# Performance work log

Hardware: AMD Instinct MI355X
Metric: run time of the kernel (lower is better)

The kernel has to match this reference:

```python
import jax, jax.numpy as jnp
import numpy as np

N, NC, E, S = 65536, 24576, 524288, 256
VAR_DIM, H1, H2, H3, H4 = 6, 128, 128, 256, 128
THRE, EPS = 0.7, 1e-5


def _bn(x, g, b):
    # BatchNorm1d, training-mode batch statistics (biased var), dropout treated as identity
    mu = x.mean(0)
    v = x.var(0)
    return (x - mu) * jax.lax.rsqrt(v + EPS) * g + b


def _gcn_sparse(h, src, dst, ew, W, b):
    # PyG GCNConv with edge weights: add self-loops (weight 1), symmetric normalization
    n = h.shape[0]
    loop = jnp.arange(n)
    s = jnp.concatenate([src, loop])
    d = jnp.concatenate([dst, loop])
    w = jnp.concatenate([ew, jnp.ones((n,), h.dtype)])
    deg = jax.ops.segment_sum(w, d, num_segments=n)
    dinv = jnp.where(deg > 0, jax.lax.rsqrt(deg), 0.0)
    norm = dinv[s] * w * dinv[d]
    xw = h @ W.T  # [n, out]
    out = jax.ops.segment_sum(norm[:, None] * xw[s], d, num_segments=n)
    return out + b


def _gcn_dense(h, A, W, b):
    # GCNConv on a dense binary adjacency (no edge weights), self-loops + sym norm
    n = h.shape[0]
    A_hat = A + jnp.eye(n, dtype=h.dtype)
    deg = A_hat.sum(0)
    dinv = jnp.where(deg > 0, jax.lax.rsqrt(deg), 0.0)
    return dinv[:, None] * (A_hat.T @ ((h @ W.T) * dinv[:, None])) + b


def setup_inputs() -> dict:
    key = jax.random.key(0)
    ks = jax.random.split(key, 10)

    def w(k, o, i):
        return jax.random.normal(k, (o, i), jnp.float32) / np.float32(np.sqrt(i))

    x = jax.random.normal(ks[0], (N, VAR_DIM), jnp.float32)
    edge_attr = jax.random.uniform(ks[1], (E,), jnp.float32)
    scen_adj = jax.random.uniform(ks[2], (S, S), jnp.float32)
    edge_index = jax.random.randint(ks[3], (2, E), 0, N)
    batch = jnp.arange(N) // (N // S)  # sorted node->graph ids, 256 nodes per graph
    mark = jnp.concatenate([jnp.ones((NC,), jnp.int32), jnp.zeros((N - NC,), jnp.int32)])
    return {
        "x": x, "edge_attr": edge_attr, "scen_adj": scen_adj,
        "mlp_var_w": w(ks[4], H1, VAR_DIM), "mlp_var_b": jnp.zeros((H1,), jnp.float32),
        "mlp_con_w": w(ks[5], H1, 1), "mlp_con_b": jnp.zeros((H1,), jnp.float32),
        "conv1_w": w(ks[6], H2, H1), "conv1_b": jnp.zeros((H2,), jnp.float32),
        "conv2_w": w(ks[7], H3, H2), "conv2_b": jnp.zeros((H3,), jnp.float32),
        "conv3_w": w(ks[8], H4, H3), "conv3_b": jnp.zeros((H4,), jnp.float32),
        "bn1_g": jnp.ones((H1,), jnp.float32), "bn1_b": jnp.zeros((H1,), jnp.float32),
        "bn2_g": jnp.ones((H2,), jnp.float32), "bn2_b": jnp.zeros((H2,), jnp.float32),
        "bn3_g": jnp.ones((H3,), jnp.float32), "bn3_b": jnp.zeros((H3,), jnp.float32),
        "mark": mark, "edge_index": edge_index, "batch": batch, "n_con": NC,
    }


def reference(x, edge_attr, scen_adj, mlp_var_w, mlp_var_b, mlp_con_w, mlp_con_b,
              conv1_w, conv1_b, conv2_w, conv2_b, conv3_w, conv3_b,
              bn1_g, bn1_b, bn2_g, bn2_b, bn3_g, bn3_b,
              mark, edge_index, batch, n_con):
    nc = int(n_con)  # mark layout: first nc nodes are constraints (mark==1), rest vars
    con_feat = jnp.tanh(x[:nc, 0:1] @ mlp_con_w.T + mlp_con_b)
    var_feat = jnp.tanh(x[nc:] @ mlp_var_w.T + mlp_var_b)
    h = jnp.concatenate([con_feat, var_feat], axis=0)  # [N, H1], con-first as in torch cat
    h = _bn(h, bn1_g, bn1_b)  # dropout = identity (eval)
    h = _gcn_sparse(h, edge_index[0], edge_index[1], edge_attr, conv1_w, conv1_b)
    h = jnp.tanh(_bn(h, bn2_g, bn2_b))
    s = scen_adj.shape[0]
    sums = jax.ops.segment_sum(h, batch, num_segments=s)
    cnt = jax.ops.segment_sum(jnp.ones((h.shape[0],), h.dtype), batch, num_segments=s)
    pooled = sums / jnp.maximum(cnt, 1.0)[:, None]  # global_mean_pool -> [S, H2]
    A = (scen_adj >= THRE).astype(h.dtype)  # filter_adj + unweighted edges
    f = jnp.tanh(_bn(_gcn_dense(pooled, A, conv2_w, conv2_b), bn3_g, bn3_b))
    feat = jnp.tanh(_gcn_dense(f, A, conv3_w, conv3_b))
    return feat, feat.mean(0)
```

## Files before the change

kernel.cpp:

```cpp
#include <hip/hip_runtime.h>
#include <hip/hip_bf16.h>
#include <cstddef>

#define N_NODES 65536
#define N_EDGES 524288
#define S_GRAPH 256
#define BN_EPS 1e-5f
#define THRE 0.7f

typedef __hip_bfloat16 bf16;
typedef unsigned int uint32;
typedef unsigned char uchar;
typedef unsigned short ushort16;
typedef __attribute__((ext_vector_type(8))) short short8;
typedef __attribute__((ext_vector_type(4))) float f32x4;

__device__ __forceinline__ float blo(uint32 u) { return __uint_as_float(u << 16); }
__device__ __forceinline__ float bhi(uint32 u) { return __uint_as_float(u & 0xffff0000u); }

__device__ __forceinline__ uint32 packbf(float a, float b)
{
    bf16 ha = __float2bfloat16(a), hb = __float2bfloat16(b);
    unsigned short ua, ub;
    __builtin_memcpy(&ua, &ha, 2); __builtin_memcpy(&ub, &hb, 2);
    return (uint32)ua | ((uint32)ub << 16);
}

__device__ __forceinline__ float ftanh(float x)
{
    float e = __builtin_amdgcn_exp2f(x * 2.8853900817779268f);
    return 1.0f - 2.0f * __builtin_amdgcn_rcpf(e + 1.0f);
}

__global__ __launch_bounds__(256) void k_mlp_hist(
    const float* __restrict__ x, const float* __restrict__ wv,
    const float* __restrict__ bv, const float* __restrict__ wc,
    const float* __restrict__ bc, const int* __restrict__ nconp,
    uint32* __restrict__ h0u, float* __restrict__ stats,
    const int* __restrict__ dst, const float* __restrict__ ew,
    uint32* __restrict__ pk32, uchar* __restrict__ rank,
    const float* __restrict__ scen, float* __restrict__ fcol,
    const float* __restrict__ w1f, uint32* __restrict__ w1bk)
{
    int t = threadIdx.x;
    int b = blockIdx.x;
    if (b < 2048) {
        int e = b * 256 + t;
        int d = dst[e];
        uint32 wfix = __float2uint_rn(ew[e] * 262144.0f);
        uint32 old = atomicAdd(&pk32[d], (1u << 24) | wfix);
        rank[e] = (uchar)(old >> 24);
        return;
    }
    if (b >= 2560) {
        if (b < 2592) {
            int r0 = (b - 2560) * 8;
            float s = 0.f;
            for (int r = r0; r < r0 + 8; r++)
                s += (scen[r * 256 + t] >= THRE) ? 1.0f : 0.0f;
            atomicAdd(&fcol[t], s);
        } else {
            const float4* w4 = (const float4*)w1f;
            uint2* wo = (uint2*)w1bk;
            #pragma unroll
            for (int it = 0; it < 16; it++) {
                int fi = it * 256 + t;
                float4 w = w4[fi];
                wo[fi] = make_uint2(packbf(w.x, w.y), packbf(w.z, w.w));
            }
        }
        return;
    }
    __shared__ float xs[128 * 6];
    __shared__ float sh[256];
    int n0 = (b - 2048) * 128;
    if (t < 192) ((float4*)xs)[t] = ((const float4*)(x + (size_t)n0 * 6))[t];
    __syncthreads();

    int nc = *nconp;
    int lane = t & 63, wave = t >> 6;
    int j0 = 2 * lane;
    const float2* wv2 = (const float2*)wv;
    float2 wa0 = wv2[j0 * 3], wa1 = wv2[j0 * 3 + 1], wa2 = wv2[j0 * 3 + 2];
    float2 wb0 = wv2[j0 * 3 + 3], wb1 = wv2[j0 * 3 + 4], wb2 = wv2[j0 * 3 + 5];
    float wc0 = wc[j0], wc1 = wc[j0 + 1], bc0 = bc[j0], bc1 = bc[j0 + 1];
    float bv0 = bv[j0], bv1 = bv[j0 + 1];

    float s0 = 0.f, ss0 = 0.f, s1 = 0.f, ss1 = 0.f;
    #pragma unroll 4
    for (int m = 0; m < 32; m++) {
        int ln = wave * 32 + m;
        int n = n0 + ln;
        const float* xr = &xs[ln * 6];
        float a0, a1;
        if (n < nc) {
            float xv = xr[0];
            a0 = xv * wc0 + bc0; a1 = xv * wc1 + bc1;
        } else {
            float x0 = xr[0], x1 = xr[1], x2 = xr[2], x3 = xr[3], x4 = xr[4], x5 = xr[5];
            a0 = bv0 + x0 * wa0.x + x1 * wa0.y + x2 * wa1.x + x3 * wa1.y + x4 * wa2.x + x5 * wa2.y;
            a1 = bv1 + x0 * wb0.x + x1 * wb0.y + x2 * wb1.x + x3 * wb1.y + x4 * wb2.x + x5 * wb2.y;
        }
        uint32 pk = packbf(ftanh(a0), ftanh(a1));
        h0u[(size_t)n * 64 + lane] = pk;
        float v0 = blo(pk), v1 = bhi(pk);
        s0 += v0; ss0 += v0 * v0; s1 += v1; ss1 += v1 * v1;
    }
    sh[t] = s0; __syncthreads();
    if (t < 64) atomicAdd(&stats[2 * t], sh[t] + sh[t + 64] + sh[t + 128] + sh[t + 192]);
    __syncthreads(); sh[t] = s1; __syncthreads();
    if (t < 64) atomicAdd(&stats[2 * t + 1], sh[t] + sh[t + 64] + sh[t + 128] + sh[t + 192]);
    __syncthreads(); sh[t] = ss0; __syncthreads();
    if (t < 64) atomicAdd(&stats[128 + 2 * t], sh[t] + sh[t + 64] + sh[t + 128] + sh[t + 192]);
    __syncthreads(); sh[t] = ss1; __syncthreads();
    if (t < 64) atomicAdd(&stats[128 + 2 * t + 1], sh[t] + sh[t + 64] + sh[t + 128] + sh[t + 192]);
}

__global__ void k_scan(const uint32* __restrict__ pk32, int* __restrict__ rowp,
                       int* __restrict__ bsum, int* __restrict__ boff,
                       float* __restrict__ deg, int* __restrict__ ctr)
{
    __shared__ int sh[256];
    __shared__ int flag;
    int b = blockIdx.x, t = threadIdx.x;
    int i = b * 256 + t;
    uint32 pv = pk32[i];
    int cnt = (int)(pv >> 24);
    int pcnt = (cnt + 3) & ~3;
    deg[i] = rsqrtf((float)(pv & 0xFFFFFFu) * 3.814697265625e-6f + 1.0f);
    sh[t] = pcnt; __syncthreads();
    for (int o = 1; o < 256; o <<= 1) {
        int u = (t >= o) ? sh[t - o] : 0;
        __syncthreads();
        sh[t] += u;
        __syncthreads();
    }
    rowp[i] = sh[t] - pcnt;
    if (t == 255) atomicExch(&bsum[b], sh[255]);
    __syncthreads();
    if (t == 0) {
        __threadfence();
        flag = (atomicAdd(ctr, 1) == 255) ? 1 : 0;
    }
    __syncthreads();
    if (flag) {
        __threadfence();
        int v = bsum[t];
        sh[t] = v; __syncthreads();
        for (int o = 1; o < 256; o <<= 1) {
            int u = (t >= o) ? sh[t - o] : 0;
            __syncthreads();
            sh[t] += u;
            __syncthreads();
        }
        boff[t] = sh[t] - v;
    }
}

__global__ __launch_bounds__(256) void k_gemm1f(
    const uint32* __restrict__ h0u, const uint32* __restrict__ w1bk,
    const float* __restrict__ g1, const float* __restrict__ bb1,
    const float* __restrict__ stats, ushort16* __restrict__ xws,
    const int* __restrict__ src, const int* __restrict__ dst,
    const float* __restrict__ ew, const float* __restrict__ dinv,
    const int* __restrict__ rowp, const int* __restrict__ boff,
    const uchar* __restrict__ rank, const uint32* __restrict__ pk32,
    int2* __restrict__ epk)
{
    int t = threadIdx.x;
    int blk = blockIdx.x;
    if (blk >= 1024) {
        if (blk < 3072) {
            int e = (blk - 1024) * 256 + t;
            int s = src[e], d = dst[e];
            int p = rowp[d] + boff[d >> 8] + (int)rank[e];
            float w = dinv[s] * ew[e] * dinv[d];
            epk[p] = make_int2(s, __float_as_int(w));
        } else {
            int n = (blk - 3072) * 256 + t;
            int st = rowp[n] + boff[n >> 8];
            int cnt = (int)(pk32[n] >> 24);
            int pcnt = (cnt + 3) & ~3;
            for (int q = cnt; q < pcnt; q++) epk[st + q] = make_int2(n, 0);
        }
        return;
    }
    __shared__ short hn_s[64 * 136];
    __shared__ short w_s[128 * 136];
    __shared__ float sc[128], sf[128];
    int row0 = blk * 64;

    if (t < 128) {
        float mu  = stats[t] * (1.0f / N_NODES);
        float var = stats[128 + t] * (1.0f / N_NODES) - mu * mu;
        float rs  = rsqrtf(fmaxf(var, 0.f) + BN_EPS);
        float s   = rs * g1[t];
        sc[t] = s;
        sf[t] = bb1[t] - mu * s;
    }
    __syncthreads();

    const uint4* h4 = (const uint4*)(h0u + (size_t)row0 * 64);
    #pragma unroll
    for (int it = 0; it < 4; it++) {
        int slot = it * 256 + t;
        int r = slot >> 4, k0 = (slot & 15) * 8;
        uint4 u = h4[slot];
        uint32 ua[4] = {u.x, u.y, u.z, u.w};
        uint32 o[4];
        #pragma unroll
        for (int m = 0; m < 4; m++) {
            int k = k0 + 2 * m;
            o[m] = packbf(blo(ua[m]) * sc[k] + sf[k], bhi(ua[m]) * sc[k + 1] + sf[k + 1]);
        }
        *(uint4*)&hn_s[r * 136 + k0] = make_uint4(o[0], o[1], o[2], o[3]);
    }
    const uint4* wv4 = (const uint4*)w1bk;
    #pragma unroll
    for (int it = 0; it < 8; it++) {
        int s2 = it * 256 + t;
        int c = s2 >> 4, k0 = (s2 & 15) * 8;
        *(uint4*)&w_s[c * 136 + k0] = wv4[s2];
    }
    __syncthreads();

    int lane = t & 63, wave = t >> 6;
    int m16 = lane & 15, kh = lane >> 4;
    int mbase = wave * 16;
    f32x4 acc[8] = {};
    #pragma unroll
    for (int ks = 0; ks < 4; ks++) {
        short8 a = *(const short8*)&hn_s[(mbase + m16) * 136 + ks * 32 + kh * 8];
        #pragma unroll
        for (int ct = 0; ct < 8; ct++) {
            short8 bfr = *(const short8*)&w_s[(ct * 16 + m16) * 136 + ks * 32 + kh * 8];
            acc[ct] = __builtin_amdgcn_mfma_f32_16x16x32_bf16(a, bfr, acc[ct], 0, 0, 0);
        }
    }
    #pragma unroll
    for (int ct = 0; ct < 8; ct++) {
        int col = ct * 16 + m16;
        #pragma unroll
        for (int r = 0; r < 4; r++) {
            int row = mbase + kh * 4 + r;
            bf16 hv = __float2bfloat16(acc[ct][r]);
            unsigned short us; __builtin_memcpy(&us, &hv, 2);
            xws[(size_t)(row0 + row) * 128 + col] = us;
        }
    }
}

__global__ void k_gather(const int* __restrict__ rowp, const int* __restrict__ boff,
                         const uint32* __restrict__ pk32, const int2* __restrict__ epk,
                         const uint32* __restrict__ xwu, const float* __restrict__ dinv,
                         const float2* __restrict__ b1c2, uint32* __restrict__ aggu)
{
    int t = threadIdx.x;
    int lane = t & 63;
    int n = blockIdx.x * 4 + (t >> 6);
    int st = rowp[n] + boff[n >> 8];
    int pcnt = (((int)(pk32[n] >> 24)) + 3) & ~3;
    float di = dinv[n];
    float d2 = di * di;
    uint32 u0 = xwu[(size_t)n * 64 + lane];
    float2 bb = b1c2[lane];
    float ax = d2 * blo(u0) + bb.x;
    float ay = d2 * bhi(u0) + bb.y;
    int en = st + pcnt;
    for (int p = st; p < en; p += 4) {
        int2 q0 = epk[p], q1 = epk[p + 1], q2 = epk[p + 2], q3 = epk[p + 3];
        uint32 v0 = xwu[(size_t)q0.x * 64 + lane];
        uint32 v1 = xwu[(size_t)q1.x * 64 + lane];
        uint32 v2 = xwu[(size_t)q2.x * 64 + lane];
        uint32 v3 = xwu[(size_t)q3.x * 64 + lane];
        float w0 = __int_as_float(q0.y), w1 = __int_as_float(q1.y);
        float w2 = __int_as_float(q2.y), w3 = __int_as_float(q3.y);
        ax += w0 * blo(v0) + w1 * blo(v1) + w2 * blo(v2) + w3 * blo(v3);
        ay += w0 * bhi(v0) + w1 * bhi(v1) + w2 * bhi(v2) + w3 * bhi(v3);
    }
    aggu[(size_t)n * 64 + lane] = packbf(ax, ay);
}

__global__ void k_colstats_bf(const uint32* __restrict__ m, float* __restrict__ stats2r)
{
    __shared__ float sh[256];
    int t = threadIdx.x, b = blockIdx.x;
    float s0 = 0.f, ss0 = 0.f, s1 = 0.f, ss1 = 0.f;
    for (int idx = b * 256 + t; idx < N_NODES * 64; idx += 1024 * 256) {
        uint32 u = m[idx];
        float a = blo(u), c = bhi(u);
        s0 += a; ss0 += a * a; s1 += c; ss1 += c * c;
    }
    float* st = stats2r + (b & 7) * 256;
    sh[t] = s0; __syncthreads();
    if (t < 64) atomicAdd(&st[2 * t], sh[t] + sh[t + 64] + sh[t + 128] + sh[t + 192]);
    __syncthreads(); sh[t] = s1; __syncthreads();
    if (t < 64) atomicAdd(&st[2 * t + 1], sh[t] + sh[t + 64] + sh[t + 128] + sh[t + 192]);
    __syncthreads(); sh[t] = ss0; __syncthreads();
    if (t < 64) atomicAdd(&st[128 + 2 * t], sh[t] + sh[t + 64] + sh[t + 128] + sh[t + 192]);
    __syncthreads(); sh[t] = ss1; __syncthreads();
    if (t < 64) atomicAdd(&st[128 + 2 * t + 1], sh[t] + sh[t + 64] + sh[t + 128] + sh[t + 192]);
}

__global__ __launch_bounds__(512) void k_poolg2(
    const uint32* __restrict__ aggu, const float* __restrict__ stats2r,
    const float* __restrict__ g2, const float* __restrict__ bb2,
    const float* __restrict__ w2, float* __restrict__ z1)
{
    __shared__ float sc[128], sf[128], sh[512], prow[128];
    int t = threadIdx.x, g = blockIdx.x;
    if (t < 128) {
        float su = 0.f, sq = 0.f;
        #pragma unroll
        for (int r = 0; r < 8; r++) {
            su += stats2r[r * 256 + t];
            sq += stats2r[r * 256 + 128 + t];
        }
        float mu  = su * (1.0f / N_NODES);
        float var = sq * (1.0f / N_NODES) - mu * mu;
        float rs  = rsqrtf(fmaxf(var, 0.f) + BN_EPS);
        float s   = rs * g2[t];
        sc[t] = s;
        sf[t] = bb2[t] - mu * s;
    }
    __syncthreads();
    int c = t & 63, grp = t >> 6;
    float c0s = sc[2 * c], c0f = sf[2 * c], c1s = sc[2 * c + 1], c1f = sf[2 * c + 1];
    const uint32* base = aggu + (size_t)g * 256 * 64;
    float s0 = 0.f, s1 = 0.f;
    for (int r = grp * 32; r < grp * 32 + 32; r++) {
        uint32 u = base[r * 64 + c];
        s0 += ftanh(blo(u) * c0s + c0f);
        s1 += ftanh(bhi(u) * c1s + c1f);
    }
    sh[t] = s0; __syncthreads();
    if (t < 64) {
        float acc = 0.f;
        #pragma unroll
        for (int k = 0; k < 8; k++) acc += sh[t + 64 * k];
        prow[2 * t] = acc * (1.0f / 256.0f);
    }
    __syncthreads(); sh[t] = s1; __syncthreads();
    if (t < 64) {
        float acc = 0.f;
        #pragma unroll
        for (int k = 0; k < 8; k++) acc += sh[t + 64 * k];
        prow[2 * t + 1] = acc * (1.0f / 256.0f);
    }
    __syncthreads();
    if (t < 256) {
        float acc = 0.f;
        const float* wr = w2 + t * 128;
        for (int k = 0; k < 128; k++) acc += prow[k] * wr[k];
        z1[g * 256 + t] = acc;
    }
}

__global__ void k_dgcn1(const float* __restrict__ scen, const float* __restrict__ fcol,
                        const float* __restrict__ z1, const float* __restrict__ b2c,
                        float* __restrict__ y1, float* __restrict__ stats3r)
{
    __shared__ float wk[256];
    int i = blockIdx.x, t = threadIdx.x;
    float a = (scen[t * 256 + i] >= THRE) ? 1.0f : 0.0f;
    if (t == i) a += 1.0f;
    wk[t] = a * rsqrtf(fcol[t] + 1.0f);
    __syncthreads();
    float acc = 0.f;
    for (int k = 0; k < 256; k++) acc += wk[k] * z1[k * 256 + t];
    float v = rsqrtf(fcol[i] + 1.0f) * acc + b2c[t];
    y1[i * 256 + t] = v;
    float* s3 = stats3r + (i & 7) * 512;
    atomicAdd(&s3[t], v);
    atomicAdd(&s3[256 + t], v * v);
}

__global__ void k_gemm3(const float* __restrict__ y1, const float* __restrict__ stats3r,
                        const float* __restrict__ g3, const float* __restrict__ bb3,
                        const float* __restrict__ w3, float* __restrict__ z2)
{
    __shared__ float row[256];
    int i = blockIdx.x, t = threadIdx.x;
    for (int c = t; c < 256; c += 128) {
        float s = 0.f, ss = 0.f;
        #pragma unroll
        for (int r = 0; r < 8; r++) {
            s  += stats3r[r * 512 + c];
            ss += stats3r[r * 512 + 256 + c];
        }
        float mu  = s * (1.0f / 256.0f);
        float var = ss * (1.0f / 256.0f) - mu * mu;
        float rs  = rsqrtf(fmaxf(var, 0.f) + BN_EPS);
        float scj = rs * g3[c];
        float sfj = bb3[c] - mu * scj;
        row[c] = ftanh(y1[i * 256 + c] * scj + sfj);
    }
    __syncthreads();
    float acc = 0.f;
    const float* wr = w3 + t * 256;
    for (int k = 0; k < 256; k++) acc += row[k] * wr[k];
    z2[i * 128 + t] = acc;
}

__global__ void k_dgcn2(const float* __restrict__ scen, const float* __restrict__ fcol,
                        const float* __restrict__ z2, const float* __restrict__ b3c,
                        float* __restrict__ out, float* __restrict__ meanr,
                        int* __restrict__ ctr)
{
    __shared__ float wk[256];
    __shared__ int flag;
    int i = blockIdx.x, t = threadIdx.x;
    for (int k = t; k < 256; k += 128) {
        float a = (scen[k * 256 + i] >= THRE) ? 1.0f : 0.0f;
        if (k == i) a += 1.0f;
        wk[k] = a * rsqrtf(fcol[k] + 1.0f);
    }
    __syncthreads();
    float acc = 0.f;
    for (int k = 0; k < 256; k++) acc += wk[k] * z2[k * 128 + t];
    float v = ftanh(rsqrtf(fcol[i] + 1.0f) * acc + b3c[t]);
    out[i * 128 + t] = v;
    atomicAdd(&meanr[(i & 7) * 128 + t], v);
    __syncthreads();
    if (t == 0) {
        __threadfence();
        flag = (atomicAdd(ctr, 1) == 255) ? 1 : 0;
    }
    __syncthreads();
    if (flag) {
        __threadfence();
        float s = 0.f;
        #pragma unroll
        for (int r = 0; r < 8; r++) s += meanr[r * 128 + t];
        out[S_GRAPH * 128 + t] = s * (1.0f / 256.0f);
    }
}

extern "C" void kernel_launch(void* const* d_in, const int* in_sizes, int n_in,
                              void* d_out, int out_size, void* d_ws, size_t ws_size,
                              hipStream_t stream)
{
    const float* x        = (const float*)d_in[0];
    const float* edge_attr= (const float*)d_in[1];
    const float* scen     = (const float*)d_in[2];
    const float* wv       = (const float*)d_in[3];
    const float* bv       = (const float*)d_in[4];
    const float* wc       = (const float*)d_in[5];
    const float* bc       = (const float*)d_in[6];
    const float* w1       = (const float*)d_in[7];
    const float* b1c      = (const float*)d_in[8];
    const float* w2       = (const float*)d_in[9];
    const float* b2c      = (const float*)d_in[10];
    const float* w3       = (const float*)d_in[11];
    const float* b3c      = (const float*)d_in[12];
    const float* g1       = (const float*)d_in[13];
    const float* bb1      = (const float*)d_in[14];
    const float* g2       = (const float*)d_in[15];
    const float* bb2      = (const float*)d_in[16];
    const float* g3       = (const float*)d_in[17];
    const float* bb3      = (const float*)d_in[18];
    const int*  ei        = (const int*)d_in[20];
    const int*  nconp     = (const int*)d_in[22];
    const int*  src = ei;
    const int*  dst = ei + N_EDGES;

    float* wsf = (float*)d_ws;
    uint32*   h0u  = (uint32*)wsf;
    uint32*   aggu = (uint32*)wsf;
    uint32*   xwu  = (uint32*)(wsf + 4194304);
    float* zb      = wsf + 8388608;
    uint32* pk32   = (uint32*)zb;
    float* stats1  = zb + 65536;
    float* stats2r = stats1 + 512;
    float* stats3r = stats2r + 2048;
    float* fcol    = stats3r + 4096;
    float* meanr   = fcol + 256;
    int*   ctrs    = (int*)(meanr + 1024);
    const int ZN   = 65536 + 512 + 2048 + 4096 + 256 + 1024 + 8;
    float* deg     = zb + ZN;
    int*   rowp    = (int*)(deg + 65536);
    int*   bsum    = rowp + 65536;
    int*   boff    = bsum + 256;
    uchar* rank    = (uchar*)(boff + 256);
    int2*  epk     = (int2*)((float*)rank + 131072);
    uint32* w1bk   = (uint32*)(epk + 720896);
    float* z1      = (float*)(w1bk + 8192);
    float* y1      = z1 + 65536;
    float* z2      = y1 + 65536;

    float* out = (float*)d_out;

    hipMemsetAsync(zb, 0, ZN * sizeof(float), stream);

    k_mlp_hist<<<2593, 256, 0, stream>>>(x, wv, bv, wc, bc, nconp, h0u, stats1,
                                         dst, edge_attr, pk32, rank,
                                         scen, fcol, w1, w1bk);
    k_scan<<<256, 256, 0, stream>>>(pk32, rowp, bsum, boff, deg, &ctrs[0]);
    k_gemm1f<<<3328, 256, 0, stream>>>(h0u, w1bk, g1, bb1, stats1, (ushort16*)xwu,
                                       src, dst, edge_attr, deg, rowp, boff,
                                       rank, pk32, epk);
    k_gather<<<N_NODES / 4, 256, 0, stream>>>(rowp, boff, pk32, epk, xwu, deg,
                                              (const float2*)b1c, aggu);
    k_colstats_bf<<<1024, 256, 0, stream>>>(aggu, stats2r);
    k_poolg2<<<S_GRAPH, 512, 0, stream>>>(aggu, stats2r, g2, bb2, w2, z1);
    k_dgcn1<<<256, 256, 0, stream>>>(scen, fcol, z1, b2c, y1, stats3r);
    k_gemm3<<<256, 128, 0, stream>>>(y1, stats3r, g3, bb3, w3, z2);
    k_dgcn2<<<256, 128, 0, stream>>>(scen, fcol, z2, b3c, out, meanr, &ctrs[1]);
}
```

Before: 274.2 us.

## Replicate degree histogram into four padded copies and vectorize edge atomics

The degree/count histogram is split into four replicas, each entry padded to a 16-byte stride, chosen by edge index mod 4. Each thread now handles four edges with vector loads of dst and weights. The scan kernel merges the replicas and stores packed per-replica prefix offsets that the scatter and gather kernels use to place edges. This is meant to cut atomic contention and block count in the histogram pass, at the cost of a much larger memset, a sparser scattered atomic footprint, and extra replica reads in the scan.

```diff
diff --git a/kernel.cpp b/kernel.cpp
--- a/kernel.cpp
+++ b/kernel.cpp
@@ -44,17 +44,25 @@
 {
     int t = threadIdx.x;
     int b = blockIdx.x;
-    if (b < 2048) {
-        int e = b * 256 + t;
-        int d = dst[e];
-        uint32 wfix = __float2uint_rn(ew[e] * 262144.0f);
-        uint32 old = atomicAdd(&pk32[d], (1u << 24) | wfix);
-        rank[e] = (uchar)(old >> 24);
+    if (b < 512) {
+        int e0 = b * 1024 + t * 4;
+        int4  d4 = *(const int4*)(dst + e0);
+        float4 w4 = *(const float4*)(ew + e0);
+        uint32 o0 = atomicAdd(&pk32[(size_t)d4.x * 4],
+                              (1u << 24) | __float2uint_rn(w4.x * 262144.0f));
+        uint32 o1 = atomicAdd(&pk32[(size_t)(65536 + d4.y) * 4],
+                              (1u << 24) | __float2uint_rn(w4.y * 262144.0f));
+        uint32 o2 = atomicAdd(&pk32[(size_t)(131072 + d4.z) * 4],
+                              (1u << 24) | __float2uint_rn(w4.z * 262144.0f));
+        uint32 o3 = atomicAdd(&pk32[(size_t)(196608 + d4.w) * 4],
+                              (1u << 24) | __float2uint_rn(w4.w * 262144.0f));
+        *(uchar4*)(rank + e0) = make_uchar4((uchar)(o0 >> 24), (uchar)(o1 >> 24),
+                                            (uchar)(o2 >> 24), (uchar)(o3 >> 24));
         return;
     }
-    if (b >= 2560) {
-        if (b < 2592) {
-            int r0 = (b - 2560) * 8;
+    if (b >= 1024) {
+        if (b < 1056) {
+            int r0 = (b - 1024) * 8;
             float s = 0.f;
             for (int r = r0; r < r0 + 8; r++)
                 s += (scen[r * 256 + t] >= THRE) ? 1.0f : 0.0f;
@@ -73,7 +81,7 @@
     }
     __shared__ float xs[128 * 6];
     __shared__ float sh[256];
-    int n0 = (b - 2048) * 128;
+    int n0 = (b - 512) * 128;
     if (t < 192) ((float4*)xs)[t] = ((const float4*)(x + (size_t)n0 * 6))[t];
     __syncthreads();
 
@@ -118,16 +126,25 @@
 
 __global__ void k_scan(const uint32* __restrict__ pk32, int* __restrict__ rowp,
                        int* __restrict__ bsum, int* __restrict__ boff,
-                       float* __restrict__ deg, int* __restrict__ ctr)
+                       float* __restrict__ deg, uint32* __restrict__ roffp,
+                       int* __restrict__ ctr)
 {
     __shared__ int sh[256];
     __shared__ int flag;
     int b = blockIdx.x, t = threadIdx.x;
     int i = b * 256 + t;
-    uint32 pv = pk32[i];
-    int cnt = (int)(pv >> 24);
+    uint32 p0 = pk32[(size_t)i * 4];
+    uint32 p1 = pk32[(size_t)(65536 + i) * 4];
+    uint32 p2 = pk32[(size_t)(131072 + i) * 4];
+    uint32 p3 = pk32[(size_t)(196608 + i) * 4];
+    int c0 = (int)(p0 >> 24), c1 = (int)(p1 >> 24);
+    int c2 = (int)(p2 >> 24), c3 = (int)(p3 >> 24);
+    int cnt = c0 + c1 + c2 + c3;
+    uint32 ws = (p0 & 0xFFFFFFu) + (p1 & 0xFFFFFFu) + (p2 & 0xFFFFFFu) + (p3 & 0xFFFFFFu);
+    deg[i] = rsqrtf((float)ws * 3.814697265625e-6f + 1.0f);
+    roffp[i] = (uint32)c0 | ((uint32)(c0 + c1) << 8) |
+               ((uint32)(c0 + c1 + c2) << 16) | ((uint32)cnt << 24);
     int pcnt = (cnt + 3) & ~3;
-    deg[i] = rsqrtf((float)(pv & 0xFFFFFFu) * 3.814697265625e-6f + 1.0f);
     sh[t] = pcnt; __syncthreads();
     for (int o = 1; o < 256; o <<= 1) {
         int u = (t >= o) ? sh[t - o] : 0;
@@ -164,7 +181,7 @@
     const int* __restrict__ src, const int* __restrict__ dst,
     const float* __restrict__ ew, const float* __restrict__ dinv,
     const int* __restrict__ rowp, const int* __restrict__ boff,
-    const uchar* __restrict__ rank, const uint32* __restrict__ pk32,
+    const uchar* __restrict__ rank, const uint32* __restrict__ roffp,
     int2* __restrict__ epk)
 {
     int t = threadIdx.x;
@@ -173,13 +190,16 @@
         if (blk < 3072) {
             int e = (blk - 1024) * 256 + t;
             int s = src[e], d = dst[e];
-            int p = rowp[d] + boff[d >> 8] + (int)rank[e];
+            uint32 ro4 = roffp[d] << 8;
+            int rep = e & 3;
+            int base = (int)((ro4 >> (rep * 8)) & 0xFFu);
+            int p = rowp[d] + boff[d >> 8] + base + (int)rank[e];
             float w = dinv[s] * ew[e] * dinv[d];
             epk[p] = make_int2(s, __float_as_int(w));
         } else {
             int n = (blk - 3072) * 256 + t;
             int st = rowp[n] + boff[n >> 8];
-            int cnt = (int)(pk32[n] >> 24);
+            int cnt = (int)(roffp[n] >> 24);
             int pcnt = (cnt + 3) & ~3;
             for (int q = cnt; q < pcnt; q++) epk[st + q] = make_int2(n, 0);
         }
@@ -251,7 +271,7 @@
 }
 
 __global__ void k_gather(const int* __restrict__ rowp, const int* __restrict__ boff,
-                         const uint32* __restrict__ pk32, const int2* __restrict__ epk,
+                         const uint32* __restrict__ roffp, const int2* __restrict__ epk,
                          const uint32* __restrict__ xwu, const float* __restrict__ dinv,
                          const float2* __restrict__ b1c2, uint32* __restrict__ aggu)
 {
@@ -259,7 +279,7 @@
     int lane = t & 63;
     int n = blockIdx.x * 4 + (t >> 6);
     int st = rowp[n] + boff[n >> 8];
-    int pcnt = (((int)(pk32[n] >> 24)) + 3) & ~3;
+    int pcnt = (((int)(roffp[n] >> 24)) + 3) & ~3;
     float di = dinv[n];
     float d2 = di * di;
     uint32 u0 = xwu[(size_t)n * 64 + lane];
@@ -470,18 +490,19 @@
     uint32*   xwu  = (uint32*)(wsf + 4194304);
     float* zb      = wsf + 8388608;
     uint32* pk32   = (uint32*)zb;
-    float* stats1  = zb + 65536;
+    float* stats1  = zb + 1048576;
     float* stats2r = stats1 + 512;
     float* stats3r = stats2r + 2048;
     float* fcol    = stats3r + 4096;
     float* meanr   = fcol + 256;
     int*   ctrs    = (int*)(meanr + 1024);
-    const int ZN   = 65536 + 512 + 2048 + 4096 + 256 + 1024 + 8;
+    const int ZN   = 1048576 + 512 + 2048 + 4096 + 256 + 1024 + 8;
     float* deg     = zb + ZN;
     int*   rowp    = (int*)(deg + 65536);
     int*   bsum    = rowp + 65536;
     int*   boff    = bsum + 256;
-    uchar* rank    = (uchar*)(boff + 256);
+    uint32* roffp  = (uint32*)(boff + 256);
+    uchar* rank    = (uchar*)(roffp + 65536);
     int2*  epk     = (int2*)((float*)rank + 131072);
     uint32* w1bk   = (uint32*)(epk + 720896);
     float* z1      = (float*)(w1bk + 8192);
@@ -492,14 +513,14 @@
 
     hipMemsetAsync(zb, 0, ZN * sizeof(float), stream);
 
-    k_mlp_hist<<<2593, 256, 0, stream>>>(x, wv, bv, wc, bc, nconp, h0u, stats1,
+    k_mlp_hist<<<1057, 256, 0, stream>>>(x, wv, bv, wc, bc, nconp, h0u, stats1,
                                          dst, edge_attr, pk32, rank,
                                          scen, fcol, w1, w1bk);
-    k_scan<<<256, 256, 0, stream>>>(pk32, rowp, bsum, boff, deg, &ctrs[0]);
+    k_scan<<<256, 256, 0, stream>>>(pk32, rowp, bsum, boff, deg, roffp, &ctrs[0]);
     k_gemm1f<<<3328, 256, 0, stream>>>(h0u, w1bk, g1, bb1, stats1, (ushort16*)xwu,
                                        src, dst, edge_attr, deg, rowp, boff,
-                                       rank, pk32, epk);
-    k_gather<<<N_NODES / 4, 256, 0, stream>>>(rowp, boff, pk32, epk, xwu, deg,
+                                       rank, roffp, epk);
+    k_gather<<<N_NODES / 4, 256, 0, stream>>>(rowp, boff, roffp, epk, xwu, deg,
                                               (const float2*)b1c, aggu);
     k_colstats_bf<<<1024, 256, 0, stream>>>(aggu, stats2r);
     k_poolg2<<<S_GRAPH, 512, 0, stream>>>(aggu, stats2r, g2, bb2, w2, z1);
```

Result: no change. 276.6 us (+0.9%).

## Build CSR via per-block bin histograms, binned scatter and LDS-local sort

Applied to the files above, without the earlier changes.

Replaces the per-edge global atomic histogram and rank array with a two-level counting sort. Edges are first binned into 256 destination groups using shared-memory histograms, scanned and scattered, then each bin builds its own CSR, degrees and normalized edge weights in LDS. The dinv[src] factor is folded into the GEMM output rows, so the edge weight only needs dinv[dst]. This trades contended random global atomics for more kernel launches and an extra pass over edge data, and it assumes at most 3072 edges per bin and source ids that fit in 16 bits.

```diff
diff --git a/kernel.cpp b/kernel.cpp
--- a/kernel.cpp
+++ b/kernel.cpp
@@ -37,24 +37,31 @@
     const float* __restrict__ bv, const float* __restrict__ wc,
     const float* __restrict__ bc, const int* __restrict__ nconp,
     uint32* __restrict__ h0u, float* __restrict__ stats,
-    const int* __restrict__ dst, const float* __restrict__ ew,
-    uint32* __restrict__ pk32, uchar* __restrict__ rank,
+    const int* __restrict__ dst, uint32* __restrict__ blkhist,
     const float* __restrict__ scen, float* __restrict__ fcol,
     const float* __restrict__ w1f, uint32* __restrict__ w1bk)
 {
+    __shared__ float xs[128 * 6];
+    __shared__ float sh[256];
+    __shared__ uint32 bh[256];
     int t = threadIdx.x;
     int b = blockIdx.x;
-    if (b < 2048) {
-        int e = b * 256 + t;
-        int d = dst[e];
-        uint32 wfix = __float2uint_rn(ew[e] * 262144.0f);
-        uint32 old = atomicAdd(&pk32[d], (1u << 24) | wfix);
-        rank[e] = (uchar)(old >> 24);
+    if (b < 512) {
+        bh[t] = 0;
+        __syncthreads();
+        int e0 = b * 1024 + t * 4;
+        int4 d4 = *(const int4*)(dst + e0);
+        atomicAdd(&bh[d4.x >> 8], 1u);
+        atomicAdd(&bh[d4.y >> 8], 1u);
+        atomicAdd(&bh[d4.z >> 8], 1u);
+        atomicAdd(&bh[d4.w >> 8], 1u);
+        __syncthreads();
+        blkhist[b * 256 + t] = bh[t];
         return;
     }
-    if (b >= 2560) {
-        if (b < 2592) {
-            int r0 = (b - 2560) * 8;
+    if (b >= 1024) {
+        if (b < 1056) {
+            int r0 = (b - 1024) * 8;
             float s = 0.f;
             for (int r = r0; r < r0 + 8; r++)
                 s += (scen[r * 256 + t] >= THRE) ? 1.0f : 0.0f;
@@ -71,9 +78,7 @@
         }
         return;
     }
-    __shared__ float xs[128 * 6];
-    __shared__ float sh[256];
-    int n0 = (b - 2048) * 128;
+    int n0 = (b - 512) * 128;
     if (t < 192) ((float4*)xs)[t] = ((const float4*)(x + (size_t)n0 * 6))[t];
     __syncthreads();
 
@@ -116,27 +121,29 @@
     if (t < 64) atomicAdd(&stats[128 + 2 * t + 1], sh[t] + sh[t + 64] + sh[t + 128] + sh[t + 192]);
 }
 
-__global__ void k_scan(const uint32* __restrict__ pk32, int* __restrict__ rowp,
-                       int* __restrict__ bsum, int* __restrict__ boff,
-                       float* __restrict__ deg, int* __restrict__ ctr)
-{
-    __shared__ int sh[256];
+__global__ __launch_bounds__(256) void k_binscan(
+    const uint32* __restrict__ blkhist, uint32* __restrict__ blkoff,
+    uint32* __restrict__ binsz, uint32* __restrict__ ubase,
+    uint32* __restrict__ pbase, int* __restrict__ ctr)
+{
+    __shared__ uint32 v[512];
+    __shared__ uint32 ps[256];
     __shared__ int flag;
-    int b = blockIdx.x, t = threadIdx.x;
-    int i = b * 256 + t;
-    uint32 pv = pk32[i];
-    int cnt = (int)(pv >> 24);
-    int pcnt = (cnt + 3) & ~3;
-    deg[i] = rsqrtf((float)(pv & 0xFFFFFFu) * 3.814697265625e-6f + 1.0f);
-    sh[t] = pcnt; __syncthreads();
+    int g = blockIdx.x, t = threadIdx.x;
+    v[t]       = blkhist[t * 256 + g];
+    v[t + 256] = blkhist[(t + 256) * 256 + g];
+    __syncthreads();
+    uint32 a0 = v[2 * t], a1 = v[2 * t + 1];
+    ps[t] = a0 + a1; __syncthreads();
     for (int o = 1; o < 256; o <<= 1) {
-        int u = (t >= o) ? sh[t - o] : 0;
+        uint32 u = (t >= o) ? ps[t - o] : 0;
         __syncthreads();
-        sh[t] += u;
+        ps[t] += u;
         __syncthreads();
     }
-    rowp[i] = sh[t] - pcnt;
-    if (t == 255) atomicExch(&bsum[b], sh[255]);
+    uint32 ex = ps[t] - (a0 + a1);
+    ((uint2*)blkoff)[g * 256 + t] = make_uint2(ex, ex + a0);
+    if (t == 255) atomicExch((int*)&binsz[g], (int)ps[255]);
     __syncthreads();
     if (t == 0) {
         __threadfence();
@@ -145,49 +152,112 @@
     __syncthreads();
     if (flag) {
         __threadfence();
-        int v = bsum[t];
-        sh[t] = v; __syncthreads();
+        uint32 s = binsz[t];
+        ps[t] = s; __syncthreads();
         for (int o = 1; o < 256; o <<= 1) {
-            int u = (t >= o) ? sh[t - o] : 0;
+            uint32 u = (t >= o) ? ps[t - o] : 0;
             __syncthreads();
-            sh[t] += u;
+            ps[t] += u;
             __syncthreads();
         }
-        boff[t] = sh[t] - v;
-    }
+        ubase[t] = ps[t] - s;
+        pbase[t] = ps[t] - s + (uint32)t * 768u;
+    }
+}
+
+__global__ __launch_bounds__(256) void k_scatter(
+    const int* __restrict__ src, const int* __restrict__ dst,
+    const float* __restrict__ ew, const uint32* __restrict__ blkoff,
+    const uint32* __restrict__ ubase, uint2* __restrict__ ebin)
+{
+    __shared__ uint32 bh[256];
+    __shared__ uint32 bo[256];
+    int b = blockIdx.x, t = threadIdx.x;
+    bh[t] = 0;
+    bo[t] = ubase[t] + blkoff[t * 512 + b];
+    __syncthreads();
+    int e0 = b * 1024 + t * 4;
+    int4 d4 = *(const int4*)(dst + e0);
+    int4 s4 = *(const int4*)(src + e0);
+    float4 w4 = *(const float4*)(ew + e0);
+    int bin; uint32 r;
+    bin = d4.x >> 8; r = atomicAdd(&bh[bin], 1u);
+    ebin[bo[bin] + r] = make_uint2((uint32)s4.x | ((uint32)(d4.x & 255) << 16), __float_as_uint(w4.x));
+    bin = d4.y >> 8; r = atomicAdd(&bh[bin], 1u);
+    ebin[bo[bin] + r] = make_uint2((uint32)s4.y | ((uint32)(d4.y & 255) << 16), __float_as_uint(w4.y));
+    bin = d4.z >> 8; r = atomicAdd(&bh[bin], 1u);
+    ebin[bo[bin] + r] = make_uint2((uint32)s4.z | ((uint32)(d4.z & 255) << 16), __float_as_uint(w4.z));
+    bin = d4.w >> 8; r = atomicAdd(&bh[bin], 1u);
+    ebin[bo[bin] + r] = make_uint2((uint32)s4.w | ((uint32)(d4.w & 255) << 16), __float_as_uint(w4.w));
+}
+
+__global__ __launch_bounds__(256) void k_csr(
+    const uint2* __restrict__ ebin, const uint32* __restrict__ binsz,
+    const uint32* __restrict__ ubase, const uint32* __restrict__ pbase,
+    float* __restrict__ dinv, int* __restrict__ rowp, int* __restrict__ cnts,
+    int2* __restrict__ epk)
+{
+    __shared__ uint2 es[3072];
+    __shared__ uint32 hist[256];
+    __shared__ int sscan[256];
+    __shared__ int rloc[256];
+    __shared__ float dlv[256];
+    int g = blockIdx.x, t = threadIdx.x;
+    int start = (int)ubase[g];
+    int sz = min((int)binsz[g], 3072);
+    int pb = (int)pbase[g];
+    hist[t] = 0;
+    __syncthreads();
+    for (int i = t; i < sz; i += 256) {
+        uint2 e = ebin[start + i];
+        int dl = (e.x >> 16) & 255;
+        uint32 wfix = __float2uint_rn(__uint_as_float(e.y) * 262144.0f);
+        uint32 h = atomicAdd(&hist[dl], (1u << 24) | wfix);
+        e.x |= (h >> 24) << 24;
+        es[i] = e;
+    }
+    __syncthreads();
+    uint32 hv = hist[t];
+    int cnt = (int)(hv >> 24);
+    float di = rsqrtf((float)(hv & 0xFFFFFFu) * 3.814697265625e-6f + 1.0f);
+    dlv[t] = di;
+    dinv[g * 256 + t] = di;
+    cnts[g * 256 + t] = cnt;
+    int pcnt = (cnt + 3) & ~3;
+    sscan[t] = pcnt; __syncthreads();
+    for (int o = 1; o < 256; o <<= 1) {
+        int u = (t >= o) ? sscan[t - o] : 0;
+        __syncthreads();
+        sscan[t] += u;
+        __syncthreads();
+    }
+    int rl = sscan[t] - pcnt;
+    rloc[t] = rl;
+    rowp[g * 256 + t] = pb + rl;
+    __syncthreads();
+    for (int i = t; i < sz; i += 256) {
+        uint2 e = es[i];
+        int s  = (int)(e.x & 0xFFFFu);
+        int dl = (int)((e.x >> 16) & 255u);
+        int r  = (int)(e.x >> 24);
+        float w = __uint_as_float(e.y) * dlv[dl];
+        epk[pb + rloc[dl] + r] = make_int2(s, __float_as_int(w));
+    }
+    int base = pb + rl;
+    for (int q = cnt; q < pcnt; q++) epk[base + q] = make_int2(g * 256 + t, 0);
 }
 
 __global__ __launch_bounds__(256) void k_gemm1f(
     const uint32* __restrict__ h0u, const uint32* __restrict__ w1bk,
     const float* __restrict__ g1, const float* __restrict__ bb1,
     const float* __restrict__ stats, ushort16* __restrict__ xws,
-    const int* __restrict__ src, const int* __restrict__ dst,
-    const float* __restrict__ ew, const float* __restrict__ dinv,
-    const int* __restrict__ rowp, const int* __restrict__ boff,
-    const uchar* __restrict__ rank, const uint32* __restrict__ pk32,
-    int2* __restrict__ epk)
-{
-    int t = threadIdx.x;
-    int blk = blockIdx.x;
-    if (blk >= 1024) {
-        if (blk < 3072) {
-            int e = (blk - 1024) * 256 + t;
-            int s = src[e], d = dst[e];
-            int p = rowp[d] + boff[d >> 8] + (int)rank[e];
-            float w = dinv[s] * ew[e] * dinv[d];
-            epk[p] = make_int2(s, __float_as_int(w));
-        } else {
-            int n = (blk - 3072) * 256 + t;
-            int st = rowp[n] + boff[n >> 8];
-            int cnt = (int)(pk32[n] >> 24);
-            int pcnt = (cnt + 3) & ~3;
-            for (int q = cnt; q < pcnt; q++) epk[st + q] = make_int2(n, 0);
-        }
-        return;
-    }
+    const float* __restrict__ dinv)
+{
     __shared__ short hn_s[64 * 136];
     __shared__ short w_s[128 * 136];
     __shared__ float sc[128], sf[128];
+    int t = threadIdx.x;
+    int blk = blockIdx.x;
     int row0 = blk * 64;
 
     if (t < 128) {
@@ -237,35 +307,37 @@
             acc[ct] = __builtin_amdgcn_mfma_f32_16x16x32_bf16(a, bfr, acc[ct], 0, 0, 0);
         }
     }
+    float dvr[4];
+    #pragma unroll
+    for (int r = 0; r < 4; r++) dvr[r] = dinv[row0 + mbase + kh * 4 + r];
     #pragma unroll
     for (int ct = 0; ct < 8; ct++) {
         int col = ct * 16 + m16;
         #pragma unroll
         for (int r = 0; r < 4; r++) {
             int row = mbase + kh * 4 + r;
-            bf16 hv = __float2bfloat16(acc[ct][r]);
+            bf16 hv = __float2bfloat16(acc[ct][r] * dvr[r]);
             unsigned short us; __builtin_memcpy(&us, &hv, 2);
             xws[(size_t)(row0 + row) * 128 + col] = us;
         }
     }
 }
 
-__global__ void k_gather(const int* __restrict__ rowp, const int* __restrict__ boff,
-                         const uint32* __restrict__ pk32, const int2* __restrict__ epk,
+__global__ void k_gather(const int* __restrict__ rowp, const int* __restrict__ cnts,
+                         const int2* __restrict__ epk,
                          const uint32* __restrict__ xwu, const float* __restrict__ dinv,
                          const float2* __restrict__ b1c2, uint32* __restrict__ aggu)
 {
     int t = threadIdx.x;
     int lane = t & 63;
     int n = blockIdx.x * 4 + (t >> 6);
-    int st = rowp[n] + boff[n >> 8];
-    int pcnt = (((int)(pk32[n] >> 24)) + 3) & ~3;
+    int st = rowp[n];
+    int pcnt = (cnts[n] + 3) & ~3;
     float di = dinv[n];
-    float d2 = di * di;
     uint32 u0 = xwu[(size_t)n * 64 + lane];
     float2 bb = b1c2[lane];
-    float ax = d2 * blo(u0) + bb.x;
-    float ay = d2 * bhi(u0) + bb.y;
+    float ax = di * blo(u0) + bb.x;
+    float ay = di * bhi(u0) + bb.y;
     int en = st + pcnt;
     for (int p = st; p < en; p += 4) {
         int2 q0 = epk[p], q1 = epk[p + 1], q2 = epk[p + 2], q3 = epk[p + 3];
@@ -469,20 +541,23 @@
     uint32*   aggu = (uint32*)wsf;
     uint32*   xwu  = (uint32*)(wsf + 4194304);
     float* zb      = wsf + 8388608;
-    uint32* pk32   = (uint32*)zb;
-    float* stats1  = zb + 65536;
-    float* stats2r = stats1 + 512;
-    float* stats3r = stats2r + 2048;
-    float* fcol    = stats3r + 4096;
-    float* meanr   = fcol + 256;
-    int*   ctrs    = (int*)(meanr + 1024);
-    const int ZN   = 65536 + 512 + 2048 + 4096 + 256 + 1024 + 8;
+    float* stats1  = zb;
+    float* stats2r = zb + 512;
+    float* stats3r = zb + 2560;
+    float* fcol    = zb + 6656;
+    float* meanr   = zb + 6912;
+    int*   ctrs    = (int*)(zb + 7936);
+    const int ZN   = 7944;
     float* deg     = zb + ZN;
     int*   rowp    = (int*)(deg + 65536);
-    int*   bsum    = rowp + 65536;
-    int*   boff    = bsum + 256;
-    uchar* rank    = (uchar*)(boff + 256);
-    int2*  epk     = (int2*)((float*)rank + 131072);
+    int*   cnts    = rowp + 65536;
+    uint32* blkhist= (uint32*)(cnts + 65536);
+    uint32* blkoff = blkhist + 131072;
+    uint32* binsz  = blkoff + 131072;
+    uint32* ubase  = binsz + 256;
+    uint32* pbase  = ubase + 256;
+    uint2* ebin    = (uint2*)(pbase + 256);
+    int2*  epk     = (int2*)(ebin + 524288);
     uint32* w1bk   = (uint32*)(epk + 720896);
     float* z1      = (float*)(w1bk + 8192);
     float* y1      = z1 + 65536;
@@ -492,14 +567,13 @@
 
     hipMemsetAsync(zb, 0, ZN * sizeof(float), stream);
 
-    k_mlp_hist<<<2593, 256, 0, stream>>>(x, wv, bv, wc, bc, nconp, h0u, stats1,
-                                         dst, edge_attr, pk32, rank,
-                                         scen, fcol, w1, w1bk);
-    k_scan<<<256, 256, 0, stream>>>(pk32, rowp, bsum, boff, deg, &ctrs[0]);
-    k_gemm1f<<<3328, 256, 0, stream>>>(h0u, w1bk, g1, bb1, stats1, (ushort16*)xwu,
-                                       src, dst, edge_attr, deg, rowp, boff,
-                                       rank, pk32, epk);
-    k_gather<<<N_NODES / 4, 256, 0, stream>>>(rowp, boff, pk32, epk, xwu, deg,
+    k_mlp_hist<<<1057, 256, 0, stream>>>(x, wv, bv, wc, bc, nconp, h0u, stats1,
+                                         dst, blkhist, scen, fcol, w1, w1bk);
+    k_binscan<<<256, 256, 0, stream>>>(blkhist, blkoff, binsz, ubase, pbase, &ctrs[0]);
+    k_scatter<<<512, 256, 0, stream>>>(src, dst, edge_attr, blkoff, ubase, ebin);
+    k_csr<<<256, 256, 0, stream>>>(ebin, binsz, ubase, pbase, deg, rowp, cnts, epk);
+    k_gemm1f<<<1024, 256, 0, stream>>>(h0u, w1bk, g1, bb1, stats1, (ushort16*)xwu, deg);
+    k_gather<<<N_NODES / 4, 256, 0, stream>>>(rowp, cnts, epk, xwu, deg,
                                               (const float2*)b1c, aggu);
     k_colstats_bf<<<1024, 256, 0, stream>>>(aggu, stats2r);
     k_poolg2<<<S_GRAPH, 512, 0, stream>>>(aggu, stats2r, g2, bb2, w2, z1);
```

New measurement: 262.5 us. 1.04x faster.
